# Kernel optimization log

Measured on AMD Instinct MI355X. Metric: run time of the kernel, lower is better.

Reference implementation:

```python
import jax, jax.numpy as jnp
import numpy as np

KLD_SCALE = 10.0
COMMITMENT_COST = 0.1


def setup_inputs() -> dict:
    key = jax.random.key(0)
    k1, k2 = jax.random.split(key)
    z = jax.random.normal(k1, (32, 2048, 64), dtype=jnp.float32)
    codebook = jax.random.normal(k2, (1024, 64), dtype=jnp.float32)
    return {"z": z, "codebook": codebook}


def reference(z, codebook):
    B, N, D = z.shape
    z_e = z.reshape(B * N, D)                          # (M, D)
    # squared euclidean distance: ||z||^2 - 2 z.E^T + ||E||^2
    dist = (
        jnp.sum(z_e * z_e, axis=1, keepdims=True)
        - 2.0 * (z_e @ codebook.T)
        + jnp.sum(codebook * codebook, axis=1)[None, :]
    )                                                  # (M, K)
    ind = jnp.argmin(dist, axis=1)                     # (M,)
    z_q = codebook[ind]                                # (M, D) gather
    latent_loss = (
        COMMITMENT_COST * jnp.mean((jax.lax.stop_gradient(z_q) - z_e) ** 2)
        + jnp.mean((z_q - jax.lax.stop_gradient(z_e)) ** 2)
    ) * KLD_SCALE
    # straight-through estimator
    z_q_st = z_e + jax.lax.stop_gradient(z_q - z_e)
    return z_q_st.reshape(B, N, D), latent_loss
```

## Files before the change

### kernel.cpp

```cpp
#include <hip/hip_runtime.h>
#include <hip/hip_bf16.h>
#include <float.h>

#define DIMS 64
#define KC 1024
#define M_TOTAL 65536
#define TAU 4e-3f

typedef __attribute__((ext_vector_type(8))) short bf16x8;
typedef __attribute__((ext_vector_type(4))) float f32x4;

#define SE_OFF   0
#define PART_OFF 1024
#define CNT_OFF  2048
#define WL_OFF   2304
#define IDX_OFF  (2304 + 65536)
#define PBH_OFF  (2304 + 2*65536)
#define PBL_OFF  (PBH_OFF + 32768)

__device__ inline short f2bf(float x) {
  union { __hip_bfloat16 h; short s; } u;
  u.h = __float2bfloat16(x);
  return u.s;
}
__device__ inline float bf2f(short x) {
  union { short s; __hip_bfloat16 h; } u;
  u.s = x;
  return __bfloat162float(u.h);
}

__global__ __launch_bounds__(256) void k_se(const float* __restrict__ cb,
                                            float* __restrict__ se,
                                            int* __restrict__ cnt) {
  if (blockIdx.x == 0 && threadIdx.x == 0) *cnt = 0;
  int k = blockIdx.x * 256 + threadIdx.x;
  const float4* p = (const float4*)(cb + (size_t)k * DIMS);
  float a0 = 0.f, a1 = 0.f, a2 = 0.f, a3 = 0.f;
#pragma unroll
  for (int i = 0; i < DIMS / 4; ++i) {
    float4 v = p[i];
    a0 = fmaf(v.x, v.x, a0);
    a1 = fmaf(v.y, v.y, a1);
    a2 = fmaf(v.z, v.z, a2);
    a3 = fmaf(v.w, v.w, a3);
  }
  se[k] = (a0 + a1) + (a2 + a3);
}

__global__ __launch_bounds__(256) void k_packB(const float* __restrict__ cb,
                                               unsigned short* __restrict__ pbh,
                                               unsigned short* __restrict__ pbl) {
  const int tid = blockIdx.x * 256 + threadIdx.x;
  const int l = tid & 63;
  const int s = (tid >> 6) & 1;
  const int tt = tid >> 7;
  const int code = tt * 16 + (l & 15);
  const int k = s * 32 + (l >> 4) * 8;
  const float* p = cb + (size_t)code * DIMS + k;
  float v[8];
  ((float4*)v)[0] = ((const float4*)p)[0];
  ((float4*)v)[1] = ((const float4*)p)[1];
  bf16x8 h, lo;
#pragma unroll
  for (int j = 0; j < 8; ++j) {
    short hj = f2bf(v[j]);
    h[j] = hj;
    lo[j] = f2bf(v[j] - bf2f(hj));
  }
  *(bf16x8*)(pbh + (size_t)tid * 8) = h;
  *(bf16x8*)(pbl + (size_t)tid * 8) = lo;
}

__global__ __launch_bounds__(256) void k_dist_mfma(const float* __restrict__ z,
                                                   const unsigned short* __restrict__ pbh,
                                                   const unsigned short* __restrict__ pbl,
                                                   const float* __restrict__ se,
                                                   int* __restrict__ idxo,
                                                   int* __restrict__ wl,
                                                   int* __restrict__ cnt) {
  const int l = threadIdx.x & 63;
  const int w = threadIdx.x >> 6;
  const int r0 = blockIdx.x * 64 + w * 16;
  const int col = l & 15;
  const int g = l >> 4;

  const float* zp = z + (size_t)(r0 + col) * DIMS + g * 8;
  bf16x8 a0h, a1h, a0l, a1l;
  {
    float v[8];
    ((float4*)v)[0] = ((const float4*)zp)[0];
    ((float4*)v)[1] = ((const float4*)zp)[1];
#pragma unroll
    for (int j = 0; j < 8; ++j) {
      short hj = f2bf(v[j]);
      a0h[j] = hj;
      a0l[j] = f2bf(v[j] - bf2f(hj));
    }
    ((float4*)v)[0] = ((const float4*)(zp + 32))[0];
    ((float4*)v)[1] = ((const float4*)(zp + 32))[1];
#pragma unroll
    for (int j = 0; j < 8; ++j) {
      short hj = f2bf(v[j]);
      a1h[j] = hj;
      a1l[j] = f2bf(v[j] - bf2f(hj));
    }
  }

  const bf16x8* pbhv = (const bf16x8*)pbh;
  const bf16x8* pblv = (const bf16x8*)pbl;
  float m1[4] = {FLT_MAX, FLT_MAX, FLT_MAX, FLT_MAX};
  float m2[4] = {FLT_MAX, FLT_MAX, FLT_MAX, FLT_MAX};
  int bt[4] = {0, 0, 0, 0};

  for (int t = 0; t < 64; ++t) {
    bf16x8 b0h = pbhv[t * 128 + l];
    bf16x8 b1h = pbhv[t * 128 + 64 + l];
    bf16x8 b0l = pblv[t * 128 + l];
    bf16x8 b1l = pblv[t * 128 + 64 + l];
    f32x4 accA = {0.f, 0.f, 0.f, 0.f};
    f32x4 accB = {0.f, 0.f, 0.f, 0.f};
    accA = __builtin_amdgcn_mfma_f32_16x16x32_bf16(a0h, b0h, accA, 0, 0, 0);
    accB = __builtin_amdgcn_mfma_f32_16x16x32_bf16(a1h, b1h, accB, 0, 0, 0);
    accA = __builtin_amdgcn_mfma_f32_16x16x32_bf16(a0h, b0l, accA, 0, 0, 0);
    accB = __builtin_amdgcn_mfma_f32_16x16x32_bf16(a1h, b1l, accB, 0, 0, 0);
    accA = __builtin_amdgcn_mfma_f32_16x16x32_bf16(a0l, b0h, accA, 0, 0, 0);
    accB = __builtin_amdgcn_mfma_f32_16x16x32_bf16(a1l, b1h, accB, 0, 0, 0);
    float sec = se[t * 16 + col];
#pragma unroll
    for (int j = 0; j < 4; ++j) {
      float d = fmaf(-2.f, accA[j] + accB[j], sec);
      bool lt = d < m1[j];
      m2[j] = fminf(m2[j], lt ? m1[j] : d);
      m1[j] = fminf(m1[j], d);
      bt[j] = lt ? t : bt[j];
    }
  }

#pragma unroll
  for (int j = 0; j < 4; ++j) {
    float m1j = m1[j], m2j = m2[j];
    int ij = bt[j] * 16 + col;
    for (int msk = 1; msk <= 8; msk <<= 1) {
      float o1 = __shfl_xor(m1j, msk);
      float o2 = __shfl_xor(m2j, msk);
      int oi = __shfl_xor(ij, msk);
      bool take = (o1 < m1j) || (o1 == m1j && oi < ij);
      float hi = take ? m1j : o1;
      m2j = fminf(fminf(m2j, o2), hi);
      m1j = take ? o1 : m1j;
      ij = take ? oi : ij;
    }
    if (col == 0) {
      int row = r0 + g * 4 + j;
      idxo[row] = ij;
      if (m2j - m1j < TAU) {
        int p = atomicAdd(cnt, 1);
        wl[p] = row;
      }
    }
  }
}

__global__ __launch_bounds__(256) void k_refine(const float* __restrict__ z,
                                                const float* __restrict__ cb,
                                                const int* __restrict__ wl,
                                                const int* __restrict__ cnt,
                                                int* __restrict__ idxo) {
  __shared__ float zz[64];
  __shared__ double sd[256];
  __shared__ int si[256];
  const int t = threadIdx.x;
  const int n = *cnt;
  for (int wi = blockIdx.x; wi < n; wi += 2048) {
    const int row = wl[wi];
    if (t < 16) ((float4*)zz)[t] = ((const float4*)(z + (size_t)row * DIMS))[t];
    __syncthreads();
    const int c0 = t * 4;
    double accd[4] = {0.0, 0.0, 0.0, 0.0};
    for (int ch = 0; ch < 4; ++ch) {
      float zr[16];
#pragma unroll
      for (int q = 0; q < 4; ++q) ((float4*)zr)[q] = ((float4*)zz)[ch * 4 + q];
#pragma unroll
      for (int cc = 0; cc < 4; ++cc) {
        const float* e = cb + (size_t)(c0 + cc) * DIMS + ch * 16;
#pragma unroll
        for (int q = 0; q < 16; ++q) {
          double df = (double)zr[q] - (double)e[q];
          accd[cc] = fma(df, df, accd[cc]);
        }
      }
    }
    double best = 1e300;
    int bi = 0;
#pragma unroll
    for (int cc = 0; cc < 4; ++cc) {
      if (accd[cc] < best) { best = accd[cc]; bi = c0 + cc; }
    }
    sd[t] = best;
    si[t] = bi;
    __syncthreads();
    for (int off = 128; off > 0; off >>= 1) {
      if (t < off) {
        double ob = sd[t + off];
        int oi = si[t + off];
        if (ob < sd[t] || (ob == sd[t] && oi < si[t])) { sd[t] = ob; si[t] = oi; }
      }
      __syncthreads();
    }
    if (t == 0) idxo[row] = si[0];
    __syncthreads();
  }
}

__global__ __launch_bounds__(256) void k_out(const float* __restrict__ z,
                                             const float* __restrict__ cb,
                                             const int* __restrict__ idxi,
                                             float* __restrict__ out,
                                             float* __restrict__ partials) {
  const int tid = blockIdx.x * 256 + threadIdx.x;
  const int row = tid >> 2;
  const int q = tid & 3;
  const int code = idxi[row];
  const float4* zp = (const float4*)(z + (size_t)row * DIMS + q * 16);
  const float4* ep = (const float4*)(cb + (size_t)code * DIMS + q * 16);
  float4* op = (float4*)(out + (size_t)row * DIMS + q * 16);
  float sse = 0.f;
#pragma unroll
  for (int i = 0; i < 4; ++i) {
    float4 v = zp[i], e = ep[i];
    float dx = e.x - v.x, dy = e.y - v.y, dz = e.z - v.z, dw = e.w - v.w;
    sse = fmaf(dx, dx, sse);
    sse = fmaf(dy, dy, sse);
    sse = fmaf(dz, dz, sse);
    sse = fmaf(dw, dw, sse);
    float4 o;
    o.x = v.x + dx;
    o.y = v.y + dy;
    o.z = v.z + dz;
    o.w = v.w + dw;
    op[i] = o;
  }
  __shared__ float sh[256];
  sh[threadIdx.x] = sse;
  __syncthreads();
  for (int off = 128; off > 0; off >>= 1) {
    if (threadIdx.x < off) sh[threadIdx.x] += sh[threadIdx.x + off];
    __syncthreads();
  }
  if (threadIdx.x == 0) partials[blockIdx.x] = sh[0];
}

__global__ __launch_bounds__(256) void k_loss(const float* __restrict__ partials,
                                              float* __restrict__ out) {
  __shared__ float sh[256];
  const int t = threadIdx.x;
  sh[t] = partials[t] + partials[t + 256] + partials[t + 512] + partials[t + 768];
  __syncthreads();
  for (int off = 128; off > 0; off >>= 1) {
    if (t < off) sh[t] += sh[t + off];
    __syncthreads();
  }
  if (t == 0) {
    out[(size_t)M_TOTAL * DIMS] = sh[0] * (11.0f / (float)((size_t)M_TOTAL * DIMS));
  }
}

extern "C" void kernel_launch(void* const* d_in, const int* in_sizes, int n_in,
                              void* d_out, int out_size, void* d_ws, size_t ws_size,
                              hipStream_t stream) {
  const float* z = (const float*)d_in[0];
  const float* cb = (const float*)d_in[1];
  float* out = (float*)d_out;
  float* ws = (float*)d_ws;

  float* se = ws + SE_OFF;
  float* partials = ws + PART_OFF;
  int* cnt = (int*)(ws + CNT_OFF);
  int* wl = (int*)(ws + WL_OFF);
  int* idx = (int*)(ws + IDX_OFF);
  unsigned short* pbh = (unsigned short*)(ws + PBH_OFF);
  unsigned short* pbl = (unsigned short*)(ws + PBL_OFF);

  k_se<<<KC / 256, 256, 0, stream>>>(cb, se, cnt);
  k_packB<<<32, 256, 0, stream>>>(cb, pbh, pbl);
  k_dist_mfma<<<M_TOTAL / 64, 256, 0, stream>>>(z, pbh, pbl, se, idx, wl, cnt);
  k_refine<<<2048, 256, 0, stream>>>(z, cb, wl, cnt, idx);
  k_out<<<1024, 256, 0, stream>>>(z, cb, idx, out, partials);
  k_loss<<<1, 256, 0, stream>>>(partials, out);
}
```

Measured before the change: 71.63 us.

## Split codebook across blocks, reuse B over two row tiles, fuse refine with output

```diff
diff --git a/kernel.cpp b/kernel.cpp
--- a/kernel.cpp
+++ b/kernel.cpp
@@ -12,11 +12,11 @@
 
 #define SE_OFF   0
 #define PART_OFF 1024
-#define CNT_OFF  2048
-#define WL_OFF   2304
-#define IDX_OFF  (2304 + 65536)
-#define PBH_OFF  (2304 + 2*65536)
+#define PBH_OFF  4096
 #define PBL_OFF  (PBH_OFF + 32768)
+#define M1_OFF   (PBL_OFF + 32768)
+#define M2_OFF   (M1_OFF + 2*65536)
+#define IDXS_OFF (M2_OFF + 2*65536)
 
 __device__ inline short f2bf(float x) {
   union { __hip_bfloat16 h; short s; } u;
@@ -29,27 +29,10 @@
   return __bfloat162float(u.h);
 }
 
-__global__ __launch_bounds__(256) void k_se(const float* __restrict__ cb,
-                                            float* __restrict__ se,
-                                            int* __restrict__ cnt) {
-  if (blockIdx.x == 0 && threadIdx.x == 0) *cnt = 0;
-  int k = blockIdx.x * 256 + threadIdx.x;
-  const float4* p = (const float4*)(cb + (size_t)k * DIMS);
-  float a0 = 0.f, a1 = 0.f, a2 = 0.f, a3 = 0.f;
-#pragma unroll
-  for (int i = 0; i < DIMS / 4; ++i) {
-    float4 v = p[i];
-    a0 = fmaf(v.x, v.x, a0);
-    a1 = fmaf(v.y, v.y, a1);
-    a2 = fmaf(v.z, v.z, a2);
-    a3 = fmaf(v.w, v.w, a3);
-  }
-  se[k] = (a0 + a1) + (a2 + a3);
-}
-
-__global__ __launch_bounds__(256) void k_packB(const float* __restrict__ cb,
-                                               unsigned short* __restrict__ pbh,
-                                               unsigned short* __restrict__ pbl) {
+__global__ __launch_bounds__(256) void k_prep(const float* __restrict__ cb,
+                                              float* __restrict__ se,
+                                              unsigned short* __restrict__ pbh,
+                                              unsigned short* __restrict__ pbl) {
   const int tid = blockIdx.x * 256 + threadIdx.x;
   const int l = tid & 63;
   const int s = (tid >> 6) & 1;
@@ -69,111 +52,177 @@
   }
   *(bf16x8*)(pbh + (size_t)tid * 8) = h;
   *(bf16x8*)(pbl + (size_t)tid * 8) = lo;
-}
-
-__global__ __launch_bounds__(256) void k_dist_mfma(const float* __restrict__ z,
-                                                   const unsigned short* __restrict__ pbh,
-                                                   const unsigned short* __restrict__ pbl,
-                                                   const float* __restrict__ se,
-                                                   int* __restrict__ idxo,
-                                                   int* __restrict__ wl,
-                                                   int* __restrict__ cnt) {
+
+  if (tid < KC) {
+    const float4* q = (const float4*)(cb + (size_t)tid * DIMS);
+    float a0 = 0.f, a1 = 0.f, a2 = 0.f, a3 = 0.f;
+#pragma unroll
+    for (int i = 0; i < DIMS / 4; ++i) {
+      float4 u = q[i];
+      a0 = fmaf(u.x, u.x, a0);
+      a1 = fmaf(u.y, u.y, a1);
+      a2 = fmaf(u.z, u.z, a2);
+      a3 = fmaf(u.w, u.w, a3);
+    }
+    se[tid] = (a0 + a1) + (a2 + a3);
+  }
+}
+
+__global__ __launch_bounds__(256, 4) void k_dist(const float* __restrict__ z,
+                                                 const unsigned short* __restrict__ pbh,
+                                                 const unsigned short* __restrict__ pbl,
+                                                 const float* __restrict__ se,
+                                                 float* __restrict__ m1o,
+                                                 float* __restrict__ m2o,
+                                                 int* __restrict__ idxo) {
   const int l = threadIdx.x & 63;
   const int w = threadIdx.x >> 6;
-  const int r0 = blockIdx.x * 64 + w * 16;
+  const int split = blockIdx.x & 1;
+  const int rb = blockIdx.x >> 1;
+  const int r0 = rb * 128 + w * 32;
   const int col = l & 15;
   const int g = l >> 4;
 
-  const float* zp = z + (size_t)(r0 + col) * DIMS + g * 8;
-  bf16x8 a0h, a1h, a0l, a1l;
-  {
-    float v[8];
-    ((float4*)v)[0] = ((const float4*)zp)[0];
-    ((float4*)v)[1] = ((const float4*)zp)[1];
-#pragma unroll
-    for (int j = 0; j < 8; ++j) {
-      short hj = f2bf(v[j]);
-      a0h[j] = hj;
-      a0l[j] = f2bf(v[j] - bf2f(hj));
-    }
-    ((float4*)v)[0] = ((const float4*)(zp + 32))[0];
-    ((float4*)v)[1] = ((const float4*)(zp + 32))[1];
-#pragma unroll
-    for (int j = 0; j < 8; ++j) {
-      short hj = f2bf(v[j]);
-      a1h[j] = hj;
-      a1l[j] = f2bf(v[j] - bf2f(hj));
-    }
-  }
-
-  const bf16x8* pbhv = (const bf16x8*)pbh;
-  const bf16x8* pblv = (const bf16x8*)pbl;
-  float m1[4] = {FLT_MAX, FLT_MAX, FLT_MAX, FLT_MAX};
-  float m2[4] = {FLT_MAX, FLT_MAX, FLT_MAX, FLT_MAX};
-  int bt[4] = {0, 0, 0, 0};
-
-  for (int t = 0; t < 64; ++t) {
-    bf16x8 b0h = pbhv[t * 128 + l];
-    bf16x8 b1h = pbhv[t * 128 + 64 + l];
-    bf16x8 b0l = pblv[t * 128 + l];
-    bf16x8 b1l = pblv[t * 128 + 64 + l];
-    f32x4 accA = {0.f, 0.f, 0.f, 0.f};
-    f32x4 accB = {0.f, 0.f, 0.f, 0.f};
-    accA = __builtin_amdgcn_mfma_f32_16x16x32_bf16(a0h, b0h, accA, 0, 0, 0);
-    accB = __builtin_amdgcn_mfma_f32_16x16x32_bf16(a1h, b1h, accB, 0, 0, 0);
-    accA = __builtin_amdgcn_mfma_f32_16x16x32_bf16(a0h, b0l, accA, 0, 0, 0);
-    accB = __builtin_amdgcn_mfma_f32_16x16x32_bf16(a1h, b1l, accB, 0, 0, 0);
-    accA = __builtin_amdgcn_mfma_f32_16x16x32_bf16(a0l, b0h, accA, 0, 0, 0);
-    accB = __builtin_amdgcn_mfma_f32_16x16x32_bf16(a1l, b1h, accB, 0, 0, 0);
-    float sec = se[t * 16 + col];
+  bf16x8 ah[2][2], al[2][2];
+#pragma unroll
+  for (int rs = 0; rs < 2; ++rs) {
+    const float* zp = z + (size_t)(r0 + rs * 16 + col) * DIMS + g * 8;
+#pragma unroll
+    for (int ks = 0; ks < 2; ++ks) {
+      float v[8];
+      ((float4*)v)[0] = ((const float4*)(zp + ks * 32))[0];
+      ((float4*)v)[1] = ((const float4*)(zp + ks * 32))[1];
+      bf16x8 h, lo;
+#pragma unroll
+      for (int j = 0; j < 8; ++j) {
+        short hj = f2bf(v[j]);
+        h[j] = hj;
+        lo[j] = f2bf(v[j] - bf2f(hj));
+      }
+      ah[rs][ks] = h;
+      al[rs][ks] = lo;
+    }
+  }
+
+  const bf16x8* ph = (const bf16x8*)pbh + (size_t)(split * 32) * 128 + l;
+  const bf16x8* pq = (const bf16x8*)pbl + (size_t)(split * 32) * 128 + l;
+  const float* sep = se + split * 512 + col;
+
+  float m1[2][4], m2[2][4];
+  int bt[2][4];
+#pragma unroll
+  for (int rs = 0; rs < 2; ++rs)
 #pragma unroll
     for (int j = 0; j < 4; ++j) {
-      float d = fmaf(-2.f, accA[j] + accB[j], sec);
-      bool lt = d < m1[j];
-      m2[j] = fminf(m2[j], lt ? m1[j] : d);
-      m1[j] = fminf(m1[j], d);
-      bt[j] = lt ? t : bt[j];
-    }
-  }
-
-#pragma unroll
-  for (int j = 0; j < 4; ++j) {
-    float m1j = m1[j], m2j = m2[j];
-    int ij = bt[j] * 16 + col;
-    for (int msk = 1; msk <= 8; msk <<= 1) {
-      float o1 = __shfl_xor(m1j, msk);
-      float o2 = __shfl_xor(m2j, msk);
-      int oi = __shfl_xor(ij, msk);
-      bool take = (o1 < m1j) || (o1 == m1j && oi < ij);
-      float hi = take ? m1j : o1;
-      m2j = fminf(fminf(m2j, o2), hi);
-      m1j = take ? o1 : m1j;
-      ij = take ? oi : ij;
-    }
-    if (col == 0) {
-      int row = r0 + g * 4 + j;
-      idxo[row] = ij;
-      if (m2j - m1j < TAU) {
-        int p = atomicAdd(cnt, 1);
-        wl[p] = row;
-      }
-    }
-  }
-}
-
-__global__ __launch_bounds__(256) void k_refine(const float* __restrict__ z,
-                                                const float* __restrict__ cb,
-                                                const int* __restrict__ wl,
-                                                const int* __restrict__ cnt,
-                                                int* __restrict__ idxo) {
+      m1[rs][j] = FLT_MAX;
+      m2[rs][j] = FLT_MAX;
+      bt[rs][j] = 0;
+    }
+
+  bf16x8 nh0 = ph[0], nh1 = ph[64], nl0 = pq[0], nl1 = pq[64];
+  for (int t = 0; t < 32; ++t) {
+    bf16x8 bh0 = nh0, bh1 = nh1, bl0 = nl0, bl1 = nl1;
+    ph += 128;
+    pq += 128;
+    nh0 = ph[0];
+    nh1 = ph[64];
+    nl0 = pq[0];
+    nl1 = pq[64];
+    const float sec = sep[t * 16];
+    f32x4 acc0 = {0.f, 0.f, 0.f, 0.f};
+    f32x4 acc1 = {0.f, 0.f, 0.f, 0.f};
+    acc0 = __builtin_amdgcn_mfma_f32_16x16x32_bf16(ah[0][0], bh0, acc0, 0, 0, 0);
+    acc1 = __builtin_amdgcn_mfma_f32_16x16x32_bf16(ah[1][0], bh0, acc1, 0, 0, 0);
+    acc0 = __builtin_amdgcn_mfma_f32_16x16x32_bf16(ah[0][1], bh1, acc0, 0, 0, 0);
+    acc1 = __builtin_amdgcn_mfma_f32_16x16x32_bf16(ah[1][1], bh1, acc1, 0, 0, 0);
+    acc0 = __builtin_amdgcn_mfma_f32_16x16x32_bf16(ah[0][0], bl0, acc0, 0, 0, 0);
+    acc1 = __builtin_amdgcn_mfma_f32_16x16x32_bf16(ah[1][0], bl0, acc1, 0, 0, 0);
+    acc0 = __builtin_amdgcn_mfma_f32_16x16x32_bf16(ah[0][1], bl1, acc0, 0, 0, 0);
+    acc1 = __builtin_amdgcn_mfma_f32_16x16x32_bf16(ah[1][1], bl1, acc1, 0, 0, 0);
+    acc0 = __builtin_amdgcn_mfma_f32_16x16x32_bf16(al[0][0], bh0, acc0, 0, 0, 0);
+    acc1 = __builtin_amdgcn_mfma_f32_16x16x32_bf16(al[1][0], bh0, acc1, 0, 0, 0);
+    acc0 = __builtin_amdgcn_mfma_f32_16x16x32_bf16(al[0][1], bh1, acc0, 0, 0, 0);
+    acc1 = __builtin_amdgcn_mfma_f32_16x16x32_bf16(al[1][1], bh1, acc1, 0, 0, 0);
+#pragma unroll
+    for (int rs = 0; rs < 2; ++rs) {
+      const f32x4 acc = rs ? acc1 : acc0;
+#pragma unroll
+      for (int j = 0; j < 4; ++j) {
+        float d = fmaf(-2.f, acc[j], sec);
+        m2[rs][j] = __builtin_amdgcn_fmed3f(d, m1[rs][j], m2[rs][j]);
+        bool lt = d < m1[rs][j];
+        bt[rs][j] = lt ? t : bt[rs][j];
+        m1[rs][j] = fminf(m1[rs][j], d);
+      }
+    }
+  }
+
+  const int c0 = split * 512;
+#pragma unroll
+  for (int rs = 0; rs < 2; ++rs)
+#pragma unroll
+    for (int j = 0; j < 4; ++j) {
+      float m1j = m1[rs][j], m2j = m2[rs][j];
+      int ij = c0 + bt[rs][j] * 16 + col;
+      for (int msk = 1; msk <= 8; msk <<= 1) {
+        float o1 = __shfl_xor(m1j, msk);
+        float o2 = __shfl_xor(m2j, msk);
+        int oi = __shfl_xor(ij, msk);
+        bool take = (o1 < m1j) || (o1 == m1j && oi < ij);
+        float hi = take ? m1j : o1;
+        m2j = fminf(fminf(m2j, o2), hi);
+        m1j = take ? o1 : m1j;
+        ij = take ? oi : ij;
+      }
+      if (col == 0) {
+        const int o = split * M_TOTAL + r0 + rs * 16 + g * 4 + j;
+        m1o[o] = m1j;
+        m2o[o] = m2j;
+        idxo[o] = ij;
+      }
+    }
+}
+
+__global__ __launch_bounds__(256) void k_fin(const float* __restrict__ z,
+                                             const float* __restrict__ cb,
+                                             const float* __restrict__ m1s,
+                                             const float* __restrict__ m2s,
+                                             const int* __restrict__ idxs,
+                                             float* __restrict__ out,
+                                             float* __restrict__ partials) {
+  const int t = threadIdx.x;
+  const int rb = blockIdx.x;
+  __shared__ int s_idx[32];
+  __shared__ int s_rows[32];
+  __shared__ int s_n;
   __shared__ float zz[64];
   __shared__ double sd[256];
   __shared__ int si[256];
-  const int t = threadIdx.x;
-  const int n = *cnt;
-  for (int wi = blockIdx.x; wi < n; wi += 2048) {
-    const int row = wl[wi];
-    if (t < 16) ((float4*)zz)[t] = ((const float4*)(z + (size_t)row * DIMS))[t];
+  __shared__ float s_sse[256];
+
+  if (t == 0) s_n = 0;
+  __syncthreads();
+
+  if (t < 32) {
+    const int row = rb * 32 + t;
+    const float a1 = m1s[row], a2 = m2s[row];
+    const float b1 = m1s[M_TOTAL + row], b2 = m2s[M_TOTAL + row];
+    const int ia = idxs[row], ib = idxs[M_TOTAL + row];
+    const float m1 = fminf(a1, b1);
+    const float m2 = fminf(fmaxf(a1, b1), fminf(a2, b2));
+    s_idx[t] = (b1 < a1) ? ib : ia;
+    if (m2 - m1 < TAU) {
+      int p = atomicAdd(&s_n, 1);
+      s_rows[p] = t;
+    }
+  }
+  __syncthreads();
+
+  const int nf = s_n;
+  for (int f = 0; f < nf; ++f) {
+    const int lrow = s_rows[f];
+    const int frow = rb * 32 + lrow;
+    if (t < 16) ((float4*)zz)[t] = ((const float4*)(z + (size_t)frow * DIMS))[t];
     __syncthreads();
     const int c0 = t * 4;
     double accd[4] = {0.0, 0.0, 0.0, 0.0};
@@ -194,9 +243,8 @@
     double best = 1e300;
     int bi = 0;
 #pragma unroll
-    for (int cc = 0; cc < 4; ++cc) {
+    for (int cc = 0; cc < 4; ++cc)
       if (accd[cc] < best) { best = accd[cc]; bi = c0 + cc; }
-    }
     sd[t] = best;
     si[t] = bi;
     __syncthreads();
@@ -208,26 +256,20 @@
       }
       __syncthreads();
     }
-    if (t == 0) idxo[row] = si[0];
-    __syncthreads();
-  }
-}
-
-__global__ __launch_bounds__(256) void k_out(const float* __restrict__ z,
-                                             const float* __restrict__ cb,
-                                             const int* __restrict__ idxi,
-                                             float* __restrict__ out,
-                                             float* __restrict__ partials) {
-  const int tid = blockIdx.x * 256 + threadIdx.x;
-  const int row = tid >> 2;
-  const int q = tid & 3;
-  const int code = idxi[row];
-  const float4* zp = (const float4*)(z + (size_t)row * DIMS + q * 16);
-  const float4* ep = (const float4*)(cb + (size_t)code * DIMS + q * 16);
-  float4* op = (float4*)(out + (size_t)row * DIMS + q * 16);
+    if (t == 0) s_idx[lrow] = si[0];
+    __syncthreads();
+  }
+
+  const int lr = t >> 3;
+  const int q = t & 7;
+  const int row = rb * 32 + lr;
+  const int code = s_idx[lr];
+  const float4* zp = (const float4*)(z + (size_t)row * DIMS + q * 8);
+  const float4* ep = (const float4*)(cb + (size_t)code * DIMS + q * 8);
+  float4* op = (float4*)(out + (size_t)row * DIMS + q * 8);
   float sse = 0.f;
 #pragma unroll
-  for (int i = 0; i < 4; ++i) {
+  for (int i = 0; i < 2; ++i) {
     float4 v = zp[i], e = ep[i];
     float dx = e.x - v.x, dy = e.y - v.y, dz = e.z - v.z, dw = e.w - v.w;
     sse = fmaf(dx, dx, sse);
@@ -241,21 +283,23 @@
     o.w = v.w + dw;
     op[i] = o;
   }
-  __shared__ float sh[256];
-  sh[threadIdx.x] = sse;
+  s_sse[t] = sse;
   __syncthreads();
   for (int off = 128; off > 0; off >>= 1) {
-    if (threadIdx.x < off) sh[threadIdx.x] += sh[threadIdx.x + off];
-    __syncthreads();
-  }
-  if (threadIdx.x == 0) partials[blockIdx.x] = sh[0];
+    if (t < off) s_sse[t] += s_sse[t + off];
+    __syncthreads();
+  }
+  if (t == 0) partials[rb] = s_sse[0];
 }
 
 __global__ __launch_bounds__(256) void k_loss(const float* __restrict__ partials,
                                               float* __restrict__ out) {
   __shared__ float sh[256];
   const int t = threadIdx.x;
-  sh[t] = partials[t] + partials[t + 256] + partials[t + 512] + partials[t + 768];
+  float s = 0.f;
+#pragma unroll
+  for (int i = 0; i < 8; ++i) s += partials[t + i * 256];
+  sh[t] = s;
   __syncthreads();
   for (int off = 128; off > 0; off >>= 1) {
     if (t < off) sh[t] += sh[t + off];
@@ -276,16 +320,14 @@
 
   float* se = ws + SE_OFF;
   float* partials = ws + PART_OFF;
-  int* cnt = (int*)(ws + CNT_OFF);
-  int* wl = (int*)(ws + WL_OFF);
-  int* idx = (int*)(ws + IDX_OFF);
   unsigned short* pbh = (unsigned short*)(ws + PBH_OFF);
   unsigned short* pbl = (unsigned short*)(ws + PBL_OFF);
-
-  k_se<<<KC / 256, 256, 0, stream>>>(cb, se, cnt);
-  k_packB<<<32, 256, 0, stream>>>(cb, pbh, pbl);
-  k_dist_mfma<<<M_TOTAL / 64, 256, 0, stream>>>(z, pbh, pbl, se, idx, wl, cnt);
-  k_refine<<<2048, 256, 0, stream>>>(z, cb, wl, cnt, idx);
-  k_out<<<1024, 256, 0, stream>>>(z, cb, idx, out, partials);
+  float* m1s = ws + M1_OFF;
+  float* m2s = ws + M2_OFF;
+  int* idxs = (int*)(ws + IDXS_OFF);
+
+  k_prep<<<32, 256, 0, stream>>>(cb, se, pbh, pbl);
+  k_dist<<<(M_TOTAL / 128) * 2, 256, 0, stream>>>(z, pbh, pbl, se, m1s, m2s, idxs);
+  k_fin<<<M_TOTAL / 32, 256, 0, stream>>>(z, cb, m1s, m2s, idxs, out, partials);
   k_loss<<<1, 256, 0, stream>>>(partials, out);
 }
```

After: 69.86 us. 1.03x faster.
